# Performance work log

Measured on AMD Instinct MI355X. Metric: run time of the kernel, lower is better.

## Reference

```python
import jax, jax.numpy as jnp
import numpy as np

DIM = 128
WIN = (7, 7)
HEADS = 4
N = WIN[0] * WIN[1]
HEAD_DIM = DIM // HEADS
SCALE = HEAD_DIM ** -0.5
NW = 64          # num windows per image
B_ = 4096        # num_windows * batch


def _relative_position_index():
    ch, cw = np.meshgrid(np.arange(WIN[0]), np.arange(WIN[1]), indexing='ij')
    coords = np.stack([ch, cw]).reshape(2, -1)          # (2, N)
    rel = coords[:, :, None] - coords[:, None, :]        # (2, N, N)
    rel = rel.transpose(1, 2, 0).astype(np.int32)
    rel[:, :, 0] += WIN[0] - 1
    rel[:, :, 1] += WIN[1] - 1
    rel[:, :, 0] *= 2 * WIN[1] - 1
    return jnp.asarray(rel.sum(-1))                      # (N, N) int32


def setup_inputs() -> dict:
    key = jax.random.key(0)
    ks = jax.random.split(key, 7)
    x = jax.random.normal(ks[0], (B_, N, DIM), dtype=jnp.float32)
    # Swin-style shifted-window mask: 0 or -100 per (window, i, j)
    mask = jnp.where(jax.random.uniform(ks[1], (NW, N, N)) < 0.1, -100.0, 0.0).astype(jnp.float32)
    qkv_w = jax.random.normal(ks[2], (3 * DIM, DIM), dtype=jnp.float32) * 0.02
    qkv_b = jnp.zeros((3 * DIM,), dtype=jnp.float32)
    proj_w = jax.random.normal(ks[3], (DIM, DIM), dtype=jnp.float32) * 0.02
    proj_b = jnp.zeros((DIM,), dtype=jnp.float32)
    bias_table = jax.random.normal(ks[4], ((2 * WIN[0] - 1) * (2 * WIN[1] - 1), HEADS), dtype=jnp.float32) * 0.02
    rel_index = _relative_position_index()
    return {"x": x, "mask": mask, "qkv_w": qkv_w, "qkv_b": qkv_b,
            "proj_w": proj_w, "proj_b": proj_b, "bias_table": bias_table,
            "rel_index": rel_index}


def reference(x, mask, qkv_w, qkv_b, proj_w, proj_b, bias_table, rel_index):
    Bw, n, c = x.shape
    # qkv projection -> (3, Bw, H, N, head_dim)
    qkv = (x @ qkv_w.T + qkv_b).reshape(Bw, n, 3, HEADS, HEAD_DIM)
    qkv = jnp.transpose(qkv, (2, 0, 3, 1, 4))
    q, k, v = qkv[0] * SCALE, qkv[1], qkv[2]
    attn = jnp.einsum('bhnd,bhmd->bhnm', q, k)           # (Bw, H, N, N)
    rel_bias = bias_table[rel_index.reshape(-1)].reshape(n, n, HEADS)
    attn = attn + jnp.transpose(rel_bias, (2, 0, 1))[None]
    nW = mask.shape[0]
    attn = attn.reshape(Bw // nW, nW, HEADS, n, n) + mask[None, :, None]
    attn = attn.reshape(Bw, HEADS, n, n)
    attn = jax.nn.softmax(attn, axis=-1)
    out = jnp.einsum('bhnm,bhmd->bhnd', attn, v)
    out = jnp.transpose(out, (0, 2, 1, 3)).reshape(Bw, n, c)
    return out @ proj_w.T + proj_b
```

## Files before the change

### kernel.cpp

```cpp
#include <hip/hip_runtime.h>

#define B_ALL 4096
#define NWIN  64
#define NTOK  49
#define DIMC  128
#define NH    4
#define HD    32
#define SCALE 0.17677669529663687f

typedef __attribute__((ext_vector_type(8))) __bf16 bf16x8;
typedef __attribute__((ext_vector_type(4))) float f32x4;


__global__ void wpack_k(const float* __restrict__ qkv_w, const float* __restrict__ proj_w,
                        __bf16* __restrict__ dst) {
  int idx = blockIdx.x * 256 + threadIdx.x;
  float w;
  __bf16 *hi, *lo;
  if (idx < 49152) { w = qkv_w[idx]; hi = dst; lo = dst + 49152; }
  else { idx -= 49152; w = proj_w[idx]; hi = dst + 98304; lo = dst + 98304 + 16384; }
  __bf16 h = (__bf16)w;
  hi[idx] = h;
  lo[idx] = (__bf16)(w - (float)h);
}

__global__ void bm_k(const float* __restrict__ mask, const float* __restrict__ bias_table,
                     const int* __restrict__ rel_index, float* __restrict__ bmT) {
  int idx = blockIdx.x * 256 + threadIdx.x;
  int i = idx % NTOK;
  int t = idx / NTOK;
  int j = t % NTOK; t /= NTOK;
  int h = t % NH;
  int wi = t / NH;
  bmT[idx] = bias_table[rel_index[i * NTOK + j] * NH + h] + mask[wi * (NTOK * NTOK) + i * NTOK + j];
}

template<int MODE>
__global__ __launch_bounds__(256)
void mgemm_k(const float* __restrict__ A, const __bf16* __restrict__ Wh,
             const __bf16* __restrict__ Wl, const float* __restrict__ bias,
             float* __restrict__ out, int M, int Bsl) {
  __shared__ __bf16 Ah[128][40], Al[128][40], Bh[128][40], Bl[128][40];
  const int tid  = threadIdx.x;
  const int lane = tid & 63, wid = tid >> 6;
  const int wrow = wid >> 1, wcol = wid & 1;
  const int mblk = blockIdx.x * 128, nblk = blockIdx.y * 128;
  const int srow = tid >> 1, skh = (tid & 1) * 16;
  const int lrow = lane & 15, lk = (lane >> 4) * 8;

  f32x4 acc[4][4];
#pragma unroll
  for (int i = 0; i < 4; ++i)
#pragma unroll
    for (int j = 0; j < 4; ++j) acc[i][j] = (f32x4){0.f, 0.f, 0.f, 0.f};

  for (int kt = 0; kt < 128; kt += 32) {
    {
      float f[16];
      int m = mblk + srow;
      if (m < M) {
        const float4* Ap = (const float4*)(A + (size_t)m * DIMC + kt + skh);
#pragma unroll
        for (int q = 0; q < 4; ++q) {
          float4 v = Ap[q];
          f[4 * q + 0] = v.x; f[4 * q + 1] = v.y; f[4 * q + 2] = v.z; f[4 * q + 3] = v.w;
        }
      } else {
#pragma unroll
        for (int e = 0; e < 16; ++e) f[e] = 0.f;
      }
      bf16x8 h0, h1, l0, l1;
#pragma unroll
      for (int e = 0; e < 8; ++e) {
        __bf16 h = (__bf16)f[e];     h0[e] = h; l0[e] = (__bf16)(f[e] - (float)h);
        __bf16 g = (__bf16)f[e + 8]; h1[e] = g; l1[e] = (__bf16)(f[e + 8] - (float)g);
      }
      *(bf16x8*)&Ah[srow][skh] = h0; *(bf16x8*)&Ah[srow][skh + 8] = h1;
      *(bf16x8*)&Al[srow][skh] = l0; *(bf16x8*)&Al[srow][skh + 8] = l1;
      const bf16x8* Whp = (const bf16x8*)(Wh + (size_t)(nblk + srow) * DIMC + kt + skh);
      const bf16x8* Wlp = (const bf16x8*)(Wl + (size_t)(nblk + srow) * DIMC + kt + skh);
      *(bf16x8*)&Bh[srow][skh] = Whp[0]; *(bf16x8*)&Bh[srow][skh + 8] = Whp[1];
      *(bf16x8*)&Bl[srow][skh] = Wlp[0]; *(bf16x8*)&Bl[srow][skh + 8] = Wlp[1];
    }
    __syncthreads();

    bf16x8 afh[4], afl[4];
#pragma unroll
    for (int mt = 0; mt < 4; ++mt) {
      afh[mt] = *(const bf16x8*)&Ah[wrow * 64 + mt * 16 + lrow][lk];
      afl[mt] = *(const bf16x8*)&Al[wrow * 64 + mt * 16 + lrow][lk];
    }
#pragma unroll
    for (int nt = 0; nt < 4; ++nt) {
      bf16x8 bh = *(const bf16x8*)&Bh[wcol * 64 + nt * 16 + lrow][lk];
      bf16x8 bl = *(const bf16x8*)&Bl[wcol * 64 + nt * 16 + lrow][lk];
#pragma unroll
      for (int mt = 0; mt < 4; ++mt) {
        acc[mt][nt] = __builtin_amdgcn_mfma_f32_16x16x32_bf16(afh[mt], bh, acc[mt][nt], 0, 0, 0);
        acc[mt][nt] = __builtin_amdgcn_mfma_f32_16x16x32_bf16(afh[mt], bl, acc[mt][nt], 0, 0, 0);
        acc[mt][nt] = __builtin_amdgcn_mfma_f32_16x16x32_bf16(afl[mt], bh, acc[mt][nt], 0, 0, 0);
      }
    }
    __syncthreads();
  }

#pragma unroll
  for (int nt = 0; nt < 4; ++nt) {
    int c = nblk + wcol * 64 + nt * 16 + lrow;
    float bv = bias[c];
#pragma unroll
    for (int mt = 0; mt < 4; ++mt) {
#pragma unroll
      for (int r = 0; r < 4; ++r) {
        int m = mblk + wrow * 64 + mt * 16 + (lane >> 4) * 4 + r;
        if (m >= M) continue;
        float v = acc[mt][nt][r] + bv;
        if (MODE == 0) {
          int s = c >> 7, hh = (c >> 5) & 3, d = c & 31;
          if (s == 0) v *= SCALE;
          int bw = m / NTOK, rr = m - bw * NTOK;
          out[((((size_t)s * Bsl + bw) * NH + hh) * NTOK + rr) * HD + d] = v;
        } else {
          out[(size_t)m * DIMC + c] = v;
        }
      }
    }
  }
}

__global__ __launch_bounds__(256, 4)
void attn_k2(const float* __restrict__ qkv, const float* __restrict__ bmT,
             float* __restrict__ attn_out, int Bsl, int win0) {
  __shared__ float kv[NH][NTOK * HD];
  const int tid = threadIdx.x;
  const int h = tid >> 6, l = tid & 63;
  const int b = blockIdx.x;
  const int wi = (win0 + b) & (NWIN - 1);

  const float4* Kh = (const float4*)(qkv + (((size_t)Bsl + b) * NH + h) * (NTOK * HD));
  float4* kvh4 = (float4*)&kv[h][0];
  for (int i = l; i < NTOK * HD / 4; i += 64) kvh4[i] = Kh[i];

  float q[HD];
  const float* Qh = qkv + ((size_t)b * NH + h) * (NTOK * HD) + l * HD;
  if (l < NTOK) {
#pragma unroll
    for (int d4 = 0; d4 < HD / 4; ++d4) {
      float4 t = ((const float4*)Qh)[d4];
      q[d4 * 4 + 0] = t.x; q[d4 * 4 + 1] = t.y; q[d4 * 4 + 2] = t.z; q[d4 * 4 + 3] = t.w;
    }
  }

  const float* bmh = bmT + ((size_t)wi * NH + h) * (NTOK * NTOK);
  float lg[NTOK];
  if (l < NTOK) {
#pragma unroll
    for (int j = 0; j < NTOK; ++j) {
      float s = bmh[j * NTOK + l];
#pragma unroll
      for (int d4 = 0; d4 < HD / 4; ++d4) {
        float4 kvec = ((const float4*)&kv[h][j * HD])[d4];
        s = fmaf(q[d4 * 4 + 0], kvec.x, s);
        s = fmaf(q[d4 * 4 + 1], kvec.y, s);
        s = fmaf(q[d4 * 4 + 2], kvec.z, s);
        s = fmaf(q[d4 * 4 + 3], kvec.w, s);
      }
      lg[j] = s;
    }
  }

  const float4* Vh = (const float4*)(qkv + (((size_t)2 * Bsl + b) * NH + h) * (NTOK * HD));
  for (int i = l; i < NTOK * HD / 4; i += 64) kvh4[i] = Vh[i];

  if (l < NTOK) {
    float mx = lg[0];
#pragma unroll
    for (int j = 1; j < NTOK; ++j) mx = fmaxf(mx, lg[j]);
    float sum = 0.f;
#pragma unroll
    for (int j = 0; j < NTOK; ++j) { float p = __expf(lg[j] - mx); lg[j] = p; sum += p; }
    float inv = 1.f / sum;

    float o[HD];
#pragma unroll
    for (int d = 0; d < HD; ++d) o[d] = 0.f;
#pragma unroll
    for (int j = 0; j < NTOK; ++j) {
      float p = lg[j];
#pragma unroll
      for (int d4 = 0; d4 < HD / 4; ++d4) {
        float4 kvec = ((const float4*)&kv[h][j * HD])[d4];
        o[d4 * 4 + 0] = fmaf(p, kvec.x, o[d4 * 4 + 0]);
        o[d4 * 4 + 1] = fmaf(p, kvec.y, o[d4 * 4 + 1]);
        o[d4 * 4 + 2] = fmaf(p, kvec.z, o[d4 * 4 + 2]);
        o[d4 * 4 + 3] = fmaf(p, kvec.w, o[d4 * 4 + 3]);
      }
    }
    float* O = attn_out + ((size_t)b * NTOK + l) * DIMC + h * HD;
#pragma unroll
    for (int d4 = 0; d4 < HD / 4; ++d4) {
      ((float4*)O)[d4] = make_float4(o[d4 * 4 + 0] * inv, o[d4 * 4 + 1] * inv,
                                     o[d4 * 4 + 2] * inv, o[d4 * 4 + 3] * inv);
    }
  }
}

extern "C" void kernel_launch(void* const* d_in, const int* in_sizes, int n_in,
                              void* d_out, int out_size, void* d_ws, size_t ws_size,
                              hipStream_t stream) {
  const float* x          = (const float*)d_in[0];
  const float* mask       = (const float*)d_in[1];
  const float* qkv_w      = (const float*)d_in[2];
  const float* qkv_b      = (const float*)d_in[3];
  const float* proj_w     = (const float*)d_in[4];
  const float* proj_b     = (const float*)d_in[5];
  const float* bias_table = (const float*)d_in[6];
  const int*   rel_index  = (const int*)d_in[7];
  float* out = (float*)d_out;

  __bf16* wpack = (__bf16*)d_ws;
  const __bf16* qwh = wpack;
  const __bf16* qwl = wpack + 49152;
  const __bf16* pwh = wpack + 98304;
  const __bf16* pwl = wpack + 98304 + 16384;
  float* bmT = (float*)((char*)d_ws + 262144);
  const size_t fixed_bytes = 262144 + 2458624;

  int NC = 1;
  while (NC < 64 && (size_t)(B_ALL / NC) * 100352ull + fixed_bytes > ws_size) NC <<= 1;
  const int Bsl = B_ALL / NC;
  const int Msl = Bsl * NTOK;

  float* qkv_ws  = (float*)((char*)d_ws + fixed_bytes);
  float* attn_ws = qkv_ws + (size_t)3 * Bsl * NH * NTOK * HD;

  wpack_k<<<dim3(256), 256, 0, stream>>>(qkv_w, proj_w, wpack);
  bm_k<<<dim3(NWIN * NH * NTOK * NTOK / 256), 256, 0, stream>>>(mask, bias_table, rel_index, bmT);

  for (int sl = 0; sl < NC; ++sl) {
    const float* xs = x + (size_t)sl * Bsl * NTOK * DIMC;
    dim3 g1((Msl + 127) / 128, 3);
    mgemm_k<0><<<g1, 256, 0, stream>>>(xs, qwh, qwl, qkv_b, qkv_ws, Msl, Bsl);
    attn_k2<<<dim3(Bsl), 256, 0, stream>>>(qkv_ws, bmT, attn_ws, Bsl, sl * Bsl);
    dim3 g3((Msl + 127) / 128, 1);
    mgemm_k<1><<<g3, 256, 0, stream>>>(attn_ws, pwh, pwl, proj_b,
                                       out + (size_t)sl * Bsl * NTOK * DIMC, Msl, Bsl);
  }
}
```

Before: 694.7 us.

## Fuse QKV projection, windowed attention, and output projection into one MFMA kernel

Replaces the three-kernel pipeline (QKV GEMM, scalar attention, projection GEMM) with one kernel per window. It computes QKV per head with split-bf16 MFMA, does QK^T and PV on MFMA with hi/lo packed operands in shared memory, and applies the output projection in the same kernel. This removes the large fp32 intermediate traffic through global memory and the scalar FMA attention loops. The bias+mask table is now padded to 64x64 with -1e9 fill. Weights are reread from global/L2 by every block rather than staged in shared memory. Limited occupancy from the large LDS footprint is a risk.

```diff
diff --git a/kernel.cpp b/kernel.cpp
--- a/kernel.cpp
+++ b/kernel.cpp
@@ -10,6 +10,9 @@
 
 typedef __attribute__((ext_vector_type(8))) __bf16 bf16x8;
 typedef __attribute__((ext_vector_type(4))) float f32x4;
+typedef __attribute__((ext_vector_type(4))) unsigned int u32x4;
+
+#define MFMA __builtin_amdgcn_mfma_f32_16x16x32_bf16
 
 
 __global__ void wpack_k(const float* __restrict__ qkv_w, const float* __restrict__ proj_w,
@@ -24,183 +27,217 @@
   lo[idx] = (__bf16)(w - (float)h);
 }
 
-__global__ void bm_k(const float* __restrict__ mask, const float* __restrict__ bias_table,
-                     const int* __restrict__ rel_index, float* __restrict__ bmT) {
+__global__ void bmf_k(const float* __restrict__ mask, const float* __restrict__ bias_table,
+                      const int* __restrict__ rel_index, float* __restrict__ bmF) {
   int idx = blockIdx.x * 256 + threadIdx.x;
-  int i = idx % NTOK;
-  int t = idx / NTOK;
-  int j = t % NTOK; t /= NTOK;
-  int h = t % NH;
-  int wi = t / NH;
-  bmT[idx] = bias_table[rel_index[i * NTOK + j] * NH + h] + mask[wi * (NTOK * NTOK) + i * NTOK + j];
-}
-
-template<int MODE>
-__global__ __launch_bounds__(256)
-void mgemm_k(const float* __restrict__ A, const __bf16* __restrict__ Wh,
-             const __bf16* __restrict__ Wl, const float* __restrict__ bias,
-             float* __restrict__ out, int M, int Bsl) {
-  __shared__ __bf16 Ah[128][40], Al[128][40], Bh[128][40], Bl[128][40];
+  int j  = idx & 63;
+  int i  = (idx >> 6) & 63;
+  int h  = (idx >> 12) & 3;
+  int wi = idx >> 14;
+  float v = -1e9f;
+  if (i < NTOK && j < NTOK)
+    v = bias_table[rel_index[i * NTOK + j] * NH + h] + mask[wi * (NTOK * NTOK) + i * NTOK + j];
+  bmF[idx] = v;
+}
+
+__device__ __forceinline__ unsigned int packsplit(float f) {
+  union { __bf16 b; unsigned short u; } H, L;
+  H.b = (__bf16)f;
+  L.b = (__bf16)(f - (float)H.b);
+  return ((unsigned int)H.u << 16) | L.u;
+}
+
+__device__ __forceinline__ void unpack_pair(const unsigned int* sp, bf16x8& hi, bf16x8& lo) {
+  union { u32x4 q[2]; unsigned int r[8]; } t;
+  t.q[0] = *(const u32x4*)sp;
+  t.q[1] = *(const u32x4*)(sp + 4);
+  union { bf16x8 v; unsigned short u[8]; } H, L;
+#pragma unroll
+  for (int e = 0; e < 8; ++e) {
+    H.u[e] = (unsigned short)(t.r[e] >> 16);
+    L.u[e] = (unsigned short)(t.r[e] & 0xffffu);
+  }
+  hi = H.v; lo = L.v;
+}
+
+__global__ __launch_bounds__(256, 2)
+void fused_k(const float* __restrict__ x,
+             const __bf16* __restrict__ qwh, const __bf16* __restrict__ qwl,
+             const float* __restrict__ qkv_b,
+             const __bf16* __restrict__ pwh, const __bf16* __restrict__ pwl,
+             const float* __restrict__ proj_b,
+             const float* __restrict__ bmF, float* __restrict__ out) {
+  __shared__ unsigned int smem[19584];
+  unsigned int* Qs = smem;
+  unsigned int* Ks = smem + 2304;
+  unsigned int* VT = smem + 4608;
+  unsigned int* Ps = smem + 6784;
+  unsigned int* AO = smem + 11136;
+
   const int tid  = threadIdx.x;
-  const int lane = tid & 63, wid = tid >> 6;
-  const int wrow = wid >> 1, wcol = wid & 1;
-  const int mblk = blockIdx.x * 128, nblk = blockIdx.y * 128;
-  const int srow = tid >> 1, skh = (tid & 1) * 16;
-  const int lrow = lane & 15, lk = (lane >> 4) * 8;
-
-  f32x4 acc[4][4];
-#pragma unroll
-  for (int i = 0; i < 4; ++i)
-#pragma unroll
-    for (int j = 0; j < 4; ++j) acc[i][j] = (f32x4){0.f, 0.f, 0.f, 0.f};
-
-  for (int kt = 0; kt < 128; kt += 32) {
+  const int lane = tid & 63, w = tid >> 6;
+  const int lrow = lane & 15, G = lane >> 4;
+  const int b = blockIdx.x, wi = b & (NWIN - 1);
+
+  bf16x8 xh[4], xl[4];
+  {
+    int row = 16 * w + lrow;
+    const float* xr = x + ((size_t)b * NTOK + (row < NTOK ? row : 0)) * DIMC;
+#pragma unroll
+    for (int ks = 0; ks < 4; ++ks) {
+      float4 a = *(const float4*)(xr + ks * 32 + 8 * G);
+      float4 c = *(const float4*)(xr + ks * 32 + 8 * G + 4);
+      float f[8] = {a.x, a.y, a.z, a.w, c.x, c.y, c.z, c.w};
+      union { bf16x8 v; __bf16 e[8]; } H, L;
+#pragma unroll
+      for (int e2 = 0; e2 < 8; ++e2) {
+        float fv = (row < NTOK) ? f[e2] : 0.f;
+        __bf16 hh = (__bf16)fv;
+        H.e[e2] = hh;
+        L.e[e2] = (__bf16)(fv - (float)hh);
+      }
+      xh[ks] = H.v; xl[ks] = L.v;
+    }
+  }
+
+#pragma unroll 1
+  for (int h = 0; h < NH; ++h) {
+    f32x4 acc[6];
+#pragma unroll
+    for (int nt = 0; nt < 6; ++nt) acc[nt] = (f32x4){0.f, 0.f, 0.f, 0.f};
+#pragma unroll
+    for (int ks = 0; ks < 4; ++ks) {
+#pragma unroll
+      for (int nt = 0; nt < 6; ++nt) {
+        int seg  = nt >> 1;
+        int wrow = seg * 128 + h * 32 + (nt & 1) * 16 + lrow;
+        bf16x8 bh = *(const bf16x8*)(qwh + (size_t)wrow * DIMC + ks * 32 + 8 * G);
+        bf16x8 bl = *(const bf16x8*)(qwl + (size_t)wrow * DIMC + ks * 32 + 8 * G);
+        acc[nt] = MFMA(xh[ks], bh, acc[nt], 0, 0, 0);
+        acc[nt] = MFMA(xh[ks], bl, acc[nt], 0, 0, 0);
+        acc[nt] = MFMA(xl[ks], bh, acc[nt], 0, 0, 0);
+      }
+    }
+#pragma unroll
+    for (int nt = 0; nt < 6; ++nt) {
+      int seg  = nt >> 1;
+      int coln = seg * 128 + h * 32 + (nt & 1) * 16 + lrow;
+      float bias = qkv_b[coln];
+      if (seg == 0) {
+#pragma unroll
+        for (int r = 0; r < 4; ++r)
+          Qs[(16 * w + 4 * G + r) * 36 + (nt & 1) * 16 + lrow] =
+              packsplit((acc[nt][r] + bias) * SCALE);
+      } else if (seg == 1) {
+#pragma unroll
+        for (int r = 0; r < 4; ++r)
+          Ks[(16 * w + 4 * G + r) * 36 + (nt & 1) * 16 + lrow] =
+              packsplit(acc[nt][r] + bias);
+      } else {
+        u32x4 pk;
+#pragma unroll
+        for (int r = 0; r < 4; ++r) pk[r] = packsplit(acc[nt][r] + bias);
+        *(u32x4*)&VT[((nt & 1) * 16 + lrow) * 68 + 16 * w + 4 * G] = pk;
+      }
+    }
+    __syncthreads();
+
+    f32x4 sa[4];
+#pragma unroll
+    for (int mt = 0; mt < 4; ++mt) sa[mt] = (f32x4){0.f, 0.f, 0.f, 0.f};
     {
-      float f[16];
-      int m = mblk + srow;
-      if (m < M) {
-        const float4* Ap = (const float4*)(A + (size_t)m * DIMC + kt + skh);
-#pragma unroll
-        for (int q = 0; q < 4; ++q) {
-          float4 v = Ap[q];
-          f[4 * q + 0] = v.x; f[4 * q + 1] = v.y; f[4 * q + 2] = v.z; f[4 * q + 3] = v.w;
-        }
-      } else {
-#pragma unroll
-        for (int e = 0; e < 16; ++e) f[e] = 0.f;
-      }
-      bf16x8 h0, h1, l0, l1;
-#pragma unroll
-      for (int e = 0; e < 8; ++e) {
-        __bf16 h = (__bf16)f[e];     h0[e] = h; l0[e] = (__bf16)(f[e] - (float)h);
-        __bf16 g = (__bf16)f[e + 8]; h1[e] = g; l1[e] = (__bf16)(f[e + 8] - (float)g);
-      }
-      *(bf16x8*)&Ah[srow][skh] = h0; *(bf16x8*)&Ah[srow][skh + 8] = h1;
-      *(bf16x8*)&Al[srow][skh] = l0; *(bf16x8*)&Al[srow][skh + 8] = l1;
-      const bf16x8* Whp = (const bf16x8*)(Wh + (size_t)(nblk + srow) * DIMC + kt + skh);
-      const bf16x8* Wlp = (const bf16x8*)(Wl + (size_t)(nblk + srow) * DIMC + kt + skh);
-      *(bf16x8*)&Bh[srow][skh] = Whp[0]; *(bf16x8*)&Bh[srow][skh + 8] = Whp[1];
-      *(bf16x8*)&Bl[srow][skh] = Wlp[0]; *(bf16x8*)&Bl[srow][skh + 8] = Wlp[1];
+      bf16x8 qbh, qbl;
+      unpack_pair(&Qs[(16 * w + lrow) * 36 + 8 * G], qbh, qbl);
+#pragma unroll
+      for (int mt = 0; mt < 4; ++mt) {
+        bf16x8 kah, kal;
+        unpack_pair(&Ks[(16 * mt + lrow) * 36 + 8 * G], kah, kal);
+        sa[mt] = MFMA(kah, qbh, sa[mt], 0, 0, 0);
+        sa[mt] = MFMA(kah, qbl, sa[mt], 0, 0, 0);
+        sa[mt] = MFMA(kal, qbh, sa[mt], 0, 0, 0);
+      }
+    }
+    float pm[4][4];
+    float mx = -3e38f;
+    const float* bmr = bmF + (((size_t)(wi * NH + h) * 64) + 16 * w + lrow) * 64;
+#pragma unroll
+    for (int mt = 0; mt < 4; ++mt) {
+      float4 bm4 = *(const float4*)(bmr + 16 * mt + 4 * G);
+      pm[mt][0] = sa[mt][0] + bm4.x;
+      pm[mt][1] = sa[mt][1] + bm4.y;
+      pm[mt][2] = sa[mt][2] + bm4.z;
+      pm[mt][3] = sa[mt][3] + bm4.w;
+#pragma unroll
+      for (int r = 0; r < 4; ++r) mx = fmaxf(mx, pm[mt][r]);
+    }
+    mx = fmaxf(mx, __shfl_xor(mx, 16));
+    mx = fmaxf(mx, __shfl_xor(mx, 32));
+    float sum = 0.f;
+#pragma unroll
+    for (int mt = 0; mt < 4; ++mt)
+#pragma unroll
+      for (int r = 0; r < 4; ++r) { pm[mt][r] = __expf(pm[mt][r] - mx); sum += pm[mt][r]; }
+    sum += __shfl_xor(sum, 16);
+    sum += __shfl_xor(sum, 32);
+    float inv = 1.f / sum;
+#pragma unroll
+    for (int mt = 0; mt < 4; ++mt) {
+      u32x4 pk;
+#pragma unroll
+      for (int r = 0; r < 4; ++r) pk[r] = packsplit(pm[mt][r]);
+      *(u32x4*)&Ps[(16 * w + lrow) * 68 + 16 * mt + 4 * G] = pk;
+    }
+    f32x4 oa[2];
+    oa[0] = (f32x4){0.f, 0.f, 0.f, 0.f};
+    oa[1] = (f32x4){0.f, 0.f, 0.f, 0.f};
+#pragma unroll
+    for (int ks2 = 0; ks2 < 2; ++ks2) {
+      bf16x8 pbh, pbl;
+      unpack_pair(&Ps[(16 * w + lrow) * 68 + ks2 * 32 + 8 * G], pbh, pbl);
+#pragma unroll
+      for (int mtd = 0; mtd < 2; ++mtd) {
+        bf16x8 vah, val_;
+        unpack_pair(&VT[(16 * mtd + lrow) * 68 + ks2 * 32 + 8 * G], vah, val_);
+        oa[mtd] = MFMA(vah, pbh, oa[mtd], 0, 0, 0);
+        oa[mtd] = MFMA(vah, pbl, oa[mtd], 0, 0, 0);
+        oa[mtd] = MFMA(val_, pbh, oa[mtd], 0, 0, 0);
+      }
+    }
+#pragma unroll
+    for (int mtd = 0; mtd < 2; ++mtd) {
+      u32x4 pk;
+#pragma unroll
+      for (int r = 0; r < 4; ++r) pk[r] = packsplit(oa[mtd][r] * inv);
+      *(u32x4*)&AO[(16 * w + lrow) * 132 + 32 * h + 16 * mtd + 4 * G] = pk;
     }
     __syncthreads();
-
-    bf16x8 afh[4], afl[4];
-#pragma unroll
-    for (int mt = 0; mt < 4; ++mt) {
-      afh[mt] = *(const bf16x8*)&Ah[wrow * 64 + mt * 16 + lrow][lk];
-      afl[mt] = *(const bf16x8*)&Al[wrow * 64 + mt * 16 + lrow][lk];
-    }
-#pragma unroll
-    for (int nt = 0; nt < 4; ++nt) {
-      bf16x8 bh = *(const bf16x8*)&Bh[wcol * 64 + nt * 16 + lrow][lk];
-      bf16x8 bl = *(const bf16x8*)&Bl[wcol * 64 + nt * 16 + lrow][lk];
-#pragma unroll
-      for (int mt = 0; mt < 4; ++mt) {
-        acc[mt][nt] = __builtin_amdgcn_mfma_f32_16x16x32_bf16(afh[mt], bh, acc[mt][nt], 0, 0, 0);
-        acc[mt][nt] = __builtin_amdgcn_mfma_f32_16x16x32_bf16(afh[mt], bl, acc[mt][nt], 0, 0, 0);
-        acc[mt][nt] = __builtin_amdgcn_mfma_f32_16x16x32_bf16(afl[mt], bh, acc[mt][nt], 0, 0, 0);
-      }
-    }
-    __syncthreads();
-  }
-
-#pragma unroll
-  for (int nt = 0; nt < 4; ++nt) {
-    int c = nblk + wcol * 64 + nt * 16 + lrow;
-    float bv = bias[c];
-#pragma unroll
-    for (int mt = 0; mt < 4; ++mt) {
-#pragma unroll
-      for (int r = 0; r < 4; ++r) {
-        int m = mblk + wrow * 64 + mt * 16 + (lane >> 4) * 4 + r;
-        if (m >= M) continue;
-        float v = acc[mt][nt][r] + bv;
-        if (MODE == 0) {
-          int s = c >> 7, hh = (c >> 5) & 3, d = c & 31;
-          if (s == 0) v *= SCALE;
-          int bw = m / NTOK, rr = m - bw * NTOK;
-          out[((((size_t)s * Bsl + bw) * NH + hh) * NTOK + rr) * HD + d] = v;
-        } else {
-          out[(size_t)m * DIMC + c] = v;
-        }
-      }
-    }
-  }
-}
-
-__global__ __launch_bounds__(256, 4)
-void attn_k2(const float* __restrict__ qkv, const float* __restrict__ bmT,
-             float* __restrict__ attn_out, int Bsl, int win0) {
-  __shared__ float kv[NH][NTOK * HD];
-  const int tid = threadIdx.x;
-  const int h = tid >> 6, l = tid & 63;
-  const int b = blockIdx.x;
-  const int wi = (win0 + b) & (NWIN - 1);
-
-  const float4* Kh = (const float4*)(qkv + (((size_t)Bsl + b) * NH + h) * (NTOK * HD));
-  float4* kvh4 = (float4*)&kv[h][0];
-  for (int i = l; i < NTOK * HD / 4; i += 64) kvh4[i] = Kh[i];
-
-  float q[HD];
-  const float* Qh = qkv + ((size_t)b * NH + h) * (NTOK * HD) + l * HD;
-  if (l < NTOK) {
-#pragma unroll
-    for (int d4 = 0; d4 < HD / 4; ++d4) {
-      float4 t = ((const float4*)Qh)[d4];
-      q[d4 * 4 + 0] = t.x; q[d4 * 4 + 1] = t.y; q[d4 * 4 + 2] = t.z; q[d4 * 4 + 3] = t.w;
-    }
-  }
-
-  const float* bmh = bmT + ((size_t)wi * NH + h) * (NTOK * NTOK);
-  float lg[NTOK];
-  if (l < NTOK) {
-#pragma unroll
-    for (int j = 0; j < NTOK; ++j) {
-      float s = bmh[j * NTOK + l];
-#pragma unroll
-      for (int d4 = 0; d4 < HD / 4; ++d4) {
-        float4 kvec = ((const float4*)&kv[h][j * HD])[d4];
-        s = fmaf(q[d4 * 4 + 0], kvec.x, s);
-        s = fmaf(q[d4 * 4 + 1], kvec.y, s);
-        s = fmaf(q[d4 * 4 + 2], kvec.z, s);
-        s = fmaf(q[d4 * 4 + 3], kvec.w, s);
-      }
-      lg[j] = s;
-    }
-  }
-
-  const float4* Vh = (const float4*)(qkv + (((size_t)2 * Bsl + b) * NH + h) * (NTOK * HD));
-  for (int i = l; i < NTOK * HD / 4; i += 64) kvh4[i] = Vh[i];
-
-  if (l < NTOK) {
-    float mx = lg[0];
-#pragma unroll
-    for (int j = 1; j < NTOK; ++j) mx = fmaxf(mx, lg[j]);
-    float sum = 0.f;
-#pragma unroll
-    for (int j = 0; j < NTOK; ++j) { float p = __expf(lg[j] - mx); lg[j] = p; sum += p; }
-    float inv = 1.f / sum;
-
-    float o[HD];
-#pragma unroll
-    for (int d = 0; d < HD; ++d) o[d] = 0.f;
-#pragma unroll
-    for (int j = 0; j < NTOK; ++j) {
-      float p = lg[j];
-#pragma unroll
-      for (int d4 = 0; d4 < HD / 4; ++d4) {
-        float4 kvec = ((const float4*)&kv[h][j * HD])[d4];
-        o[d4 * 4 + 0] = fmaf(p, kvec.x, o[d4 * 4 + 0]);
-        o[d4 * 4 + 1] = fmaf(p, kvec.y, o[d4 * 4 + 1]);
-        o[d4 * 4 + 2] = fmaf(p, kvec.z, o[d4 * 4 + 2]);
-        o[d4 * 4 + 3] = fmaf(p, kvec.w, o[d4 * 4 + 3]);
-      }
-    }
-    float* O = attn_out + ((size_t)b * NTOK + l) * DIMC + h * HD;
-#pragma unroll
-    for (int d4 = 0; d4 < HD / 4; ++d4) {
-      ((float4*)O)[d4] = make_float4(o[d4 * 4 + 0] * inv, o[d4 * 4 + 1] * inv,
-                                     o[d4 * 4 + 2] * inv, o[d4 * 4 + 3] * inv);
+  }
+
+  f32x4 pacc[8];
+#pragma unroll
+  for (int nt2 = 0; nt2 < 8; ++nt2) pacc[nt2] = (f32x4){0.f, 0.f, 0.f, 0.f};
+#pragma unroll
+  for (int ks = 0; ks < 4; ++ks) {
+    bf16x8 aah, aal;
+    unpack_pair(&AO[(16 * w + lrow) * 132 + ks * 32 + 8 * G], aah, aal);
+#pragma unroll
+    for (int nt2 = 0; nt2 < 8; ++nt2) {
+      int wr = nt2 * 16 + lrow;
+      bf16x8 bh = *(const bf16x8*)(pwh + (size_t)wr * DIMC + ks * 32 + 8 * G);
+      bf16x8 bl = *(const bf16x8*)(pwl + (size_t)wr * DIMC + ks * 32 + 8 * G);
+      pacc[nt2] = MFMA(aah, bh, pacc[nt2], 0, 0, 0);
+      pacc[nt2] = MFMA(aah, bl, pacc[nt2], 0, 0, 0);
+      pacc[nt2] = MFMA(aal, bh, pacc[nt2], 0, 0, 0);
+    }
+  }
+#pragma unroll
+  for (int nt2 = 0; nt2 < 8; ++nt2) {
+    int cp = nt2 * 16 + lrow;
+    float pb = proj_b[cp];
+#pragma unroll
+    for (int r = 0; r < 4; ++r) {
+      int mrow = 16 * w + 4 * G + r;
+      if (mrow < NTOK) out[((size_t)b * NTOK + mrow) * DIMC + cp] = pacc[nt2][r] + pb;
     }
   }
 }
@@ -223,27 +260,9 @@
   const __bf16* qwl = wpack + 49152;
   const __bf16* pwh = wpack + 98304;
   const __bf16* pwl = wpack + 98304 + 16384;
-  float* bmT = (float*)((char*)d_ws + 262144);
-  const size_t fixed_bytes = 262144 + 2458624;
-
-  int NC = 1;
-  while (NC < 64 && (size_t)(B_ALL / NC) * 100352ull + fixed_bytes > ws_size) NC <<= 1;
-  const int Bsl = B_ALL / NC;
-  const int Msl = Bsl * NTOK;
-
-  float* qkv_ws  = (float*)((char*)d_ws + fixed_bytes);
-  float* attn_ws = qkv_ws + (size_t)3 * Bsl * NH * NTOK * HD;
+  float* bmF = (float*)((char*)d_ws + 262144);
 
   wpack_k<<<dim3(256), 256, 0, stream>>>(qkv_w, proj_w, wpack);
-  bm_k<<<dim3(NWIN * NH * NTOK * NTOK / 256), 256, 0, stream>>>(mask, bias_table, rel_index, bmT);
-
-  for (int sl = 0; sl < NC; ++sl) {
-    const float* xs = x + (size_t)sl * Bsl * NTOK * DIMC;
-    dim3 g1((Msl + 127) / 128, 3);
-    mgemm_k<0><<<g1, 256, 0, stream>>>(xs, qwh, qwl, qkv_b, qkv_ws, Msl, Bsl);
-    attn_k2<<<dim3(Bsl), 256, 0, stream>>>(qkv_ws, bmT, attn_ws, Bsl, sl * Bsl);
-    dim3 g3((Msl + 127) / 128, 1);
-    mgemm_k<1><<<g3, 256, 0, stream>>>(attn_ws, pwh, pwl, proj_b,
-                                       out + (size_t)sl * Bsl * NTOK * DIMC, Msl, Bsl);
-  }
-}
+  bmf_k<<<dim3(4096), 256, 0, stream>>>(mask, bias_table, rel_index, bmF);
+  fused_k<<<dim3(B_ALL), 256, 0, stream>>>(x, qwh, qwl, qkv_b, pwh, pwl, proj_b, bmF, out);
+}
```

New measurement: 718.4 us. 3.4% more time.
